# Performance work log

Hardware: AMD Instinct MI355X
Metric: run time of the kernel (lower is better)

## Reference

```python
import jax, jax.numpy as jnp
import numpy as np

N_E = 2048
E_DIM = 64
BETA = 0.25


def _l2_normalize(x, eps=1e-12):
    # matches F.normalize: x / clamp_min(||x||, eps)
    n = jnp.linalg.norm(x, axis=-1, keepdims=True)
    return x / jnp.maximum(n, eps)


def _cosine_sim(a, b, eps=1e-8):
    # matches torch.cosine_similarity(dim=-1)
    na = jnp.maximum(jnp.linalg.norm(a, axis=-1), eps)
    nb = jnp.maximum(jnp.linalg.norm(b, axis=-1), eps)
    return jnp.sum(a * b, axis=-1) / (na * nb)


def setup_inputs() -> dict:
    key = jax.random.key(0)
    k1, k2 = jax.random.split(key)
    z = jax.random.normal(k1, (16, 64, 64, E_DIM), dtype=jnp.float32)
    bound = 1.0 / np.sqrt(E_DIM)
    emb = jax.random.uniform(k2, (N_E, E_DIM), dtype=jnp.float32,
                             minval=-bound, maxval=bound)
    return {"z": z, "emb": emb}


def reference(z, emb):
    n_e, e_dim = emb.shape
    zf = z.reshape(-1, e_dim)                      # (N, C)
    N = zf.shape[0]

    cb = _l2_normalize(emb)                        # normalized codebook (n_e, C)
    # _d normalizes cb again (idempotent) and normalizes z
    z_norm = _l2_normalize(zf)
    d = jnp.matmul(z_norm, cb.T)                   # (N, n_e) cosine similarities

    idx = jnp.argmax(d, axis=1)                    # (N,)
    probs = jax.nn.softmax(d, axis=1)              # (N, n_e)

    # one-hot @ cb == gather
    z_q = cb[idx].reshape(z.shape)

    # commitment loss (stop-gradient semantics; forward value identical)
    sg = jax.lax.stop_gradient
    commit_loss = (1.0 - jnp.mean(_cosine_sim(z_q, sg(z)))) \
        + BETA * (1.0 - jnp.mean(_cosine_sim(sg(z_q), z)))

    # e_mean = mean of one-hot encodings == normalized codeword counts
    e_mean = jnp.zeros((n_e,), dtype=z.dtype).at[idx].add(1.0) / N

    p = jnp.mean(probs, axis=0)                    # (n_e,)
    kl_loss = jnp.sum(p * (jnp.log(p) - jnp.log(1.0 / n_e)))
    load_balancing_loss = jnp.sum(e_mean * p)

    z_q_st = z + sg(z_q - z)
    perplexity = jnp.exp(-jnp.sum(e_mean * jnp.log(e_mean + 1e-6)))

    return (z_q_st, commit_loss, kl_loss, load_balancing_loss, cb, perplexity)
```

## Files before the change

kernel.cpp:

```cpp
#include <hip/hip_runtime.h>
#include <math.h>

#define NROWS 65536
#define ED 64
#define NE 2048
#define TAU 3e-4f
#define LOG2E 1.44269504089f
#define LN2 0.69314718056f
#define TAUS (TAU * LOG2E)

typedef _Float16 f16x8 __attribute__((ext_vector_type(8)));
typedef float f32x4 __attribute__((ext_vector_type(4)));

#if __has_builtin(__builtin_amdgcn_exp2f)
__device__ __forceinline__ float fexp2(float x) { return __builtin_amdgcn_exp2f(x); }
#else
__device__ __forceinline__ float fexp2(float x) {
    float r;
    asm("v_exp_f32 %0, %1" : "=v"(r) : "v"(x));
    return r;
}
#endif

#define WS_CBH      0
#define WS_CBT      65536
#define WS_RINV     196608
#define WS_MROW     262144
#define WS_IDX      327680
#define WS_FLAGCNT  393216
#define WS_COUNTS   393232
#define WS_FLAGLIST 395280
#define WS_PSUM     460816
#define WS_MPART    462864
#define WS_PPART    462928

#define OUT_ZQ     0
#define OUT_COMMIT 4194304
#define OUT_KL     4194305
#define OUT_LB     4194306
#define OUT_CB     4194307
#define OUT_PERP   4325379

#define ZS_ZNORM   0
#define ZS_PM      2097152
#define ZS_PAUX    3145728
#define ZS_PSH     3670016

__global__ void k_cb(const float* __restrict__ emb, _Float16* __restrict__ cbh,
                     float* __restrict__ cbo, float* __restrict__ cbT) {
    int t = blockIdx.x * blockDim.x + threadIdx.x;
    int row = t >> 6;
    int lane = t & 63;
    if (row >= NE) return;
    float v = emb[row * ED + lane];
    float sq = v * v;
#pragma unroll
    for (int off = 32; off > 0; off >>= 1) sq += __shfl_xor(sq, off);
    float c = v * (1.0f / fmaxf(sqrtf(sq), 1e-12f));
    cbo[row * ED + lane] = c;
    cbh[row * ED + lane] = (_Float16)c;
    cbT[(size_t)lane * NE + row] = c;
}

__global__ void k_prep(const float* __restrict__ z, _Float16* __restrict__ znorm) {
    const int tid = threadIdx.x;
    const int lane = tid & 63;
    const int w = tid >> 6;
    const int row = blockIdx.x * 64 + w * 16 + (lane >> 2);
    const int q = lane & 3;
    const float4* zp = (const float4*)(z + (size_t)row * ED + q * 16);
    const float4 a = zp[0], b = zp[1], c = zp[2], d = zp[3];
    float sq = a.x*a.x + a.y*a.y + a.z*a.z + a.w*a.w
             + b.x*b.x + b.y*b.y + b.z*b.z + b.w*b.w
             + c.x*c.x + c.y*c.y + c.z*c.z + c.w*c.w
             + d.x*d.x + d.y*d.y + d.z*d.z + d.w*d.w;
    sq += __shfl_xor(sq, 1);
    sq += __shfl_xor(sq, 2);
    const float r = LOG2E / fmaxf(sqrtf(sq), 1e-12f);
    f16x8 h0, h1;
    h0[0]=(_Float16)(a.x*r); h0[1]=(_Float16)(a.y*r); h0[2]=(_Float16)(a.z*r); h0[3]=(_Float16)(a.w*r);
    h0[4]=(_Float16)(b.x*r); h0[5]=(_Float16)(b.y*r); h0[6]=(_Float16)(b.z*r); h0[7]=(_Float16)(b.w*r);
    h1[0]=(_Float16)(c.x*r); h1[1]=(_Float16)(c.y*r); h1[2]=(_Float16)(c.z*r); h1[3]=(_Float16)(c.w*r);
    h1[4]=(_Float16)(d.x*r); h1[5]=(_Float16)(d.y*r); h1[6]=(_Float16)(d.z*r); h1[7]=(_Float16)(d.w*r);
    f16x8* dst = (f16x8*)(znorm + (size_t)row * ED + q * 16);
    dst[0] = h0; dst[1] = h1;
}

__launch_bounds__(256, 3)
__global__ void k_s1(const _Float16* __restrict__ znorm, const _Float16* __restrict__ cbh,
                     float* __restrict__ pm, unsigned short* __restrict__ paux,
                     _Float16* __restrict__ psh) {
    const int tid = threadIdx.x;
    const int lane = tid & 63;
    const int w = tid >> 6;
    const int l15 = lane & 15;
    const int lg = lane >> 4;
    const int gw = blockIdx.x * 4 + w;
    const int g = gw & 15;
    const int split = gw >> 4;
    const int cwbase = g * 128;

    f16x8 af[8][2];
#pragma unroll
    for (int jf = 0; jf < 8; ++jf) {
        const _Float16* ap = cbh + (size_t)(cwbase + jf * 16 + l15) * ED + lg * 8;
        af[jf][0] = *(const f16x8*)(ap);
        af[jf][1] = *(const f16x8*)(ap + 32);
    }

    for (int t = 0; t < 4; ++t) {
        const int rbA = split * 128 + t * 32;
        const _Float16* bpA = znorm + (size_t)(rbA + l15) * ED + lg * 8;
        const _Float16* bpB = bpA + 16 * ED;
        const f16x8 bA0 = *(const f16x8*)(bpA);
        const f16x8 bA1 = *(const f16x8*)(bpA + 32);
        const f16x8 bB0 = *(const f16x8*)(bpB);
        const f16x8 bB1 = *(const f16x8*)(bpB + 32);
        float mA = -4.f, m2A = -4.f, sA0 = 0.f, sA1 = 0.f;
        float mB = -4.f, m2B = -4.f, sB0 = 0.f, sB1 = 0.f;
        int miA = 0, miB = 0;
#pragma unroll
        for (int jf = 0; jf < 8; ++jf) {
            f32x4 cA = (f32x4){0.f, 0.f, 0.f, 0.f};
            cA = __builtin_amdgcn_mfma_f32_16x16x32_f16(af[jf][0], bA0, cA, 0, 0, 0);
            cA = __builtin_amdgcn_mfma_f32_16x16x32_f16(af[jf][1], bA1, cA, 0, 0, 0);
            f32x4 cB = (f32x4){0.f, 0.f, 0.f, 0.f};
            cB = __builtin_amdgcn_mfma_f32_16x16x32_f16(af[jf][0], bB0, cB, 0, 0, 0);
            cB = __builtin_amdgcn_mfma_f32_16x16x32_f16(af[jf][1], bB1, cB, 0, 0, 0);
            const int cw0 = cwbase + jf * 16 + lg * 4;
#pragma unroll
            for (int i = 0; i < 4; ++i) {
                const float vA = cA[i];
                m2A = fmaxf(m2A, fminf(vA, mA));
                miA = (vA > mA) ? (cw0 + i) : miA;
                mA  = fmaxf(vA, mA);
                const float vB = cB[i];
                m2B = fmaxf(m2B, fminf(vB, mB));
                miB = (vB > mB) ? (cw0 + i) : miB;
                mB  = fmaxf(vB, mB);
                if (i & 1) { sA1 += fexp2(vA); sB1 += fexp2(vB); }
                else       { sA0 += fexp2(vA); sB0 += fexp2(vB); }
            }
        }
        float sA = sA0 + sA1, sB = sB0 + sB1;
#pragma unroll
        for (int d = 16; d <= 32; d <<= 1) {
            float om = __shfl_xor(mA, d);
            float om2 = __shfl_xor(m2A, d);
            int   oi = __shfl_xor(miA, d);
            sA += __shfl_xor(sA, d);
            float nm2 = fmaxf(fmaxf(m2A, om2), fminf(mA, om));
            bool take = (om > mA) || (om == mA && oi < miA);
            miA = take ? oi : miA;  mA = take ? om : mA;  m2A = nm2;
            om = __shfl_xor(mB, d);
            om2 = __shfl_xor(m2B, d);
            oi = __shfl_xor(miB, d);
            sB += __shfl_xor(sB, d);
            nm2 = fmaxf(fmaxf(m2B, om2), fminf(mB, om));
            take = (om > mB) || (om == mB && oi < miB);
            miB = take ? oi : miB;  mB = take ? om : mB;  m2B = nm2;
        }
        if (lane < 16) {
            int row = rbA + lane;
            pm[(size_t)g * NROWS + row] = mA;
            paux[(size_t)g * NROWS + row] =
                (unsigned short)(((mA - m2A < TAUS) ? 2048 : 0) | miA);
            psh[(size_t)g * NROWS + row] = (_Float16)sA;
            row += 16;
            pm[(size_t)g * NROWS + row] = mB;
            paux[(size_t)g * NROWS + row] =
                (unsigned short)(((mB - m2B < TAUS) ? 2048 : 0) | miB);
            psh[(size_t)g * NROWS + row] = (_Float16)sB;
        }
    }
}

__global__ void k_comb(const float* __restrict__ pm, const unsigned short* __restrict__ paux,
                       const _Float16* __restrict__ psh, float* __restrict__ rinv,
                       float* __restrict__ mrow, int* __restrict__ idxw,
                       int* __restrict__ flagcnt, int* __restrict__ flaglist,
                       float* __restrict__ counts) {
    const int row = blockIdx.x * 256 + threadIdx.x;
    float mg[16];
    unsigned short ax[16];
    float s = 0.f;
#pragma unroll
    for (int g = 0; g < 16; ++g) {
        mg[g] = pm[(size_t)g * NROWS + row];
        ax[g] = paux[(size_t)g * NROWS + row];
        s += (float)psh[(size_t)g * NROWS + row];
    }
    float bm = -4.f; int bi = 0;
#pragma unroll
    for (int g = 0; g < 16; ++g) {
        if (mg[g] > bm) { bm = mg[g]; bi = ax[g] & 2047; }
    }
    int near = 0; bool fl = false;
#pragma unroll
    for (int g = 0; g < 16; ++g) {
        const bool nr = (mg[g] >= bm - TAUS);
        near += nr ? 1 : 0;
        fl = fl || (nr && (ax[g] & 2048));
    }
    rinv[row] = 1.0f / s;
    mrow[row] = bm * LN2;
    idxw[row] = bi;
    if (fl || near >= 2) {
        int e = atomicAdd(flagcnt, 1);
        flaglist[e] = row;
    } else {
        atomicAdd(&counts[bi], 1.0f);
    }
}

__launch_bounds__(256, 3)
__global__ void k_s2(const _Float16* __restrict__ znorm, const _Float16* __restrict__ cbh,
                     const float* __restrict__ rinv, float* __restrict__ ppart) {
    const int tid = threadIdx.x;
    const int lane = tid & 63;
    const int w = tid >> 6;
    const int l15 = lane & 15;
    const int lg = lane >> 4;
    const int gw = blockIdx.x * 4 + w;
    const int cwg = gw & 31;
    const int split = gw >> 5;

    f16x8 bf[4][2];
#pragma unroll
    for (int jf = 0; jf < 4; ++jf) {
        const _Float16* bp = cbh + (size_t)(cwg * 64 + jf * 16 + l15) * ED + lg * 8;
        bf[jf][0] = *(const f16x8*)(bp);
        bf[jf][1] = *(const f16x8*)(bp + 32);
    }
    float pc[4] = {0.f, 0.f, 0.f, 0.f};

    for (int t = 0; t < 32; ++t) {
        const int rowbase = split * 512 + t * 16;
        const _Float16* ap = znorm + (size_t)(rowbase + l15) * ED + lg * 8;
        const f16x8 a0 = *(const f16x8*)(ap);
        const f16x8 a1 = *(const f16x8*)(ap + 32);
        const int r0 = rowbase + lg * 4;
        const float rv0 = rinv[r0], rv1 = rinv[r0 + 1];
        const float rv2 = rinv[r0 + 2], rv3 = rinv[r0 + 3];
#pragma unroll
        for (int jf = 0; jf < 4; ++jf) {
            f32x4 c = (f32x4){0.f, 0.f, 0.f, 0.f};
            c = __builtin_amdgcn_mfma_f32_16x16x32_f16(a0, bf[jf][0], c, 0, 0, 0);
            c = __builtin_amdgcn_mfma_f32_16x16x32_f16(a1, bf[jf][1], c, 0, 0, 0);
            pc[jf] += fexp2(c[0]) * rv0 + fexp2(c[1]) * rv1
                    + fexp2(c[2]) * rv2 + fexp2(c[3]) * rv3;
        }
    }
#pragma unroll
    for (int jf = 0; jf < 4; ++jf) {
        pc[jf] += __shfl_xor(pc[jf], 16);
        pc[jf] += __shfl_xor(pc[jf], 32);
    }
    if (lg == 0) {
        float* pp = ppart + (size_t)split * NE + cwg * 64;
#pragma unroll
        for (int jf = 0; jf < 4; ++jf) pp[jf * 16 + l15] = pc[jf];
    }
}

__global__ void k_zqg(const float* __restrict__ cb32, const int* __restrict__ idxw,
                      float* __restrict__ zq) {
    const int r = blockIdx.x * 16 + (threadIdx.x >> 4);
    const int q = threadIdx.x & 15;
    const int j = idxw[r];
    ((float4*)(zq + (size_t)r * ED))[q] = ((const float4*)(cb32 + (size_t)j * ED))[q];
}

__launch_bounds__(256, 2)
__global__ void k_recheck(const float* __restrict__ z, const float* __restrict__ cbT,
                          const float* __restrict__ cb32,
                          const int* __restrict__ flagcnt, const int* __restrict__ flaglist,
                          float* __restrict__ mrow, float* __restrict__ counts,
                          float* __restrict__ zq) {
    __shared__ float zn[8][ED];
    __shared__ int   rowids[8];
    __shared__ float rbv[8][4];
    __shared__ int   rbi[8][4];
    const int n = *flagcnt;
    const int tid = threadIdx.x, lane = tid & 63, wv = tid >> 6;
    for (int base = blockIdx.x * 8; base < n; base += 512 * 8) {
#pragma unroll
        for (int rr = wv * 2; rr < wv * 2 + 2; ++rr) {
            const int e = base + rr;
            int row = -1;
            float v = 0.f;
            if (e < n) { row = flaglist[e]; v = z[(size_t)row * ED + lane]; }
            float sq = v * v;
#pragma unroll
            for (int d = 32; d > 0; d >>= 1) sq += __shfl_xor(sq, d);
            zn[rr][lane] = v * (1.0f / fmaxf(sqrtf(sq), 1e-12f));
            if (lane == 0) rowids[rr] = row;
        }
        __syncthreads();
        float acc[8][8];
#pragma unroll
        for (int r = 0; r < 8; ++r)
#pragma unroll
            for (int q = 0; q < 8; ++q) acc[r][q] = 0.f;
        for (int k = 0; k < ED; ++k) {
            float cv[8];
            const float* cr = cbT + (size_t)k * NE + tid;
#pragma unroll
            for (int q = 0; q < 8; ++q) cv[q] = cr[q * 256];
#pragma unroll
            for (int r = 0; r < 8; ++r) {
                const float zk = zn[r][k];
#pragma unroll
                for (int q = 0; q < 8; ++q)
                    acc[r][q] = fmaf(zk, cv[q], acc[r][q]);
            }
        }
#pragma unroll
        for (int r = 0; r < 8; ++r) {
            float best = -2.f; int bj = 0;
#pragma unroll
            for (int q = 0; q < 8; ++q) {
                const float vv = acc[r][q];
                const int j = q * 256 + tid;
                bj = (vv > best) ? j : bj;
                best = fmaxf(vv, best);
            }
#pragma unroll
            for (int d = 1; d < 64; d <<= 1) {
                const float o = __shfl_xor(best, d);
                const int oj = __shfl_xor(bj, d);
                const bool tk = (o > best) || (o == best && oj < bj);
                best = tk ? o : best;
                bj = tk ? oj : bj;
            }
            if (lane == 0) { rbv[r][wv] = best; rbi[r][wv] = bj; }
        }
        __syncthreads();
        if (wv == 0 && lane < 8) {
            const int r = lane;
            float bv = rbv[r][0]; int bj = rbi[r][0];
#pragma unroll
            for (int u = 1; u < 4; ++u) {
                const float o = rbv[r][u]; const int oj = rbi[r][u];
                const bool tk = (o > bv) || (o == bv && oj < bj);
                bv = tk ? o : bv; bj = tk ? oj : bj;
            }
            rbi[r][0] = bj;
            const int row = rowids[r];
            if (row >= 0) {
                mrow[row] = bv;
                atomicAdd(&counts[bj], 1.0f);
            }
        }
        __syncthreads();
#pragma unroll
        for (int rr = wv * 2; rr < wv * 2 + 2; ++rr) {
            const int row = rowids[rr];
            if (row >= 0) {
                const int bj = rbi[rr][0];
                zq[(size_t)row * ED + lane] = cb32[(size_t)bj * ED + lane];
            }
        }
    }
}

__global__ void k_red(const float* __restrict__ ppart, const float* __restrict__ mrow,
                      float* __restrict__ psum, float* __restrict__ mpart) {
    const int tid = threadIdx.x;
    if (blockIdx.x < 8) {
        const int col = blockIdx.x * 256 + tid;
        float s = 0.f;
        for (int sl = 0; sl < 128; ++sl) s += ppart[(size_t)sl * NE + col];
        psum[col] = s;
    } else {
        __shared__ float lds[4];
        const int b = blockIdx.x - 8;
        const int r0 = b * 1024;
        float s = 0.f;
        for (int r = r0 + tid; r < r0 + 1024; r += 256) s += mrow[r];
        const int lane = tid & 63, wv = tid >> 6;
#pragma unroll
        for (int d = 32; d > 0; d >>= 1) s += __shfl_xor(s, d);
        if (lane == 0) lds[wv] = s;
        __syncthreads();
        if (tid == 0) mpart[b] = lds[0] + lds[1] + lds[2] + lds[3];
    }
}

__device__ __forceinline__ float block_reduce_1024(float v, float* lds, int lane, int wid) {
#pragma unroll
    for (int off = 32; off > 0; off >>= 1) v += __shfl_xor(v, off);
    if (lane == 0) lds[wid] = v;
    __syncthreads();
    float r = 0.f;
    if (wid == 0) {
        r = (lane < 16) ? lds[lane] : 0.f;
#pragma unroll
        for (int off = 8; off > 0; off >>= 1) r += __shfl_xor(r, off);
    }
    __syncthreads();
    return r;
}

__global__ void k_final(const float* __restrict__ counts, const float* __restrict__ psum,
                        const float* __restrict__ mpart, float* __restrict__ out) {
    __shared__ float lds[16];
    const int tid = threadIdx.x;
    const int lane = tid & 63, wid = tid >> 6;
    float sm = (tid < 64) ? mpart[tid] : 0.f;
    float kl = 0.f, lb = 0.f, H = 0.f;
    const float LOGNE = logf((float)NE);
    for (int j = tid; j < NE; j += 1024) {
        const float p = psum[j] * (1.0f / NROWS);
        const float em = counts[j] * (1.0f / NROWS);
        kl += p * (logf(p) + LOGNE);
        lb += em * p;
        H += em * logf(em + 1e-6f);
    }
    sm = block_reduce_1024(sm, lds, lane, wid);
    kl = block_reduce_1024(kl, lds, lane, wid);
    lb = block_reduce_1024(lb, lds, lane, wid);
    H  = block_reduce_1024(H,  lds, lane, wid);
    if (tid == 0) {
        out[OUT_COMMIT] = 1.25f * (1.0f - sm * (1.0f / NROWS));
        out[OUT_KL] = kl;
        out[OUT_LB] = lb;
        out[OUT_PERP] = expf(-H);
    }
}

extern "C" void kernel_launch(void* const* d_in, const int* in_sizes, int n_in,
                              void* d_out, int out_size, void* d_ws, size_t ws_size,
                              hipStream_t stream) {
    const float* z   = (const float*)d_in[0];
    const float* emb = (const float*)d_in[1];
    float* out = (float*)d_out;
    float* ws  = (float*)d_ws;

    _Float16* cbh  = (_Float16*)(ws + WS_CBH);
    float* cbT     = ws + WS_CBT;
    float* rinv    = ws + WS_RINV;
    float* mrowp   = ws + WS_MROW;
    int* idxw      = (int*)(ws + WS_IDX);
    int* flagcnt   = (int*)(ws + WS_FLAGCNT);
    int* flaglist  = (int*)(ws + WS_FLAGLIST);
    float* counts  = ws + WS_COUNTS;
    float* psum    = ws + WS_PSUM;
    float* mpart   = ws + WS_MPART;
    float* ppart   = ws + WS_PPART;
    float* cb32    = out + OUT_CB;
    float* zq      = out + OUT_ZQ;

    _Float16* znorm      = (_Float16*)(zq + ZS_ZNORM);
    float* pm            = zq + ZS_PM;
    unsigned short* paux = (unsigned short*)(zq + ZS_PAUX);
    _Float16* psh        = (_Float16*)(zq + ZS_PSH);

    hipMemsetAsync(flagcnt, 0, (16 + NE) * sizeof(float), stream);

    k_cb      <<<512, 256, 0, stream>>>(emb, cbh, cb32, cbT);
    k_prep    <<<1024, 256, 0, stream>>>(z, znorm);
    k_s1      <<<2048, 256, 0, stream>>>(znorm, cbh, pm, paux, psh);
    k_comb    <<<256, 256, 0, stream>>>(pm, paux, psh, rinv, mrowp, idxw,
                                        flagcnt, flaglist, counts);
    k_s2      <<<1024, 256, 0, stream>>>(znorm, cbh, rinv, ppart);
    k_zqg     <<<4096, 256, 0, stream>>>(cb32, idxw, zq);
    k_recheck <<<512, 256, 0, stream>>>(z, cbT, cb32, flagcnt, flaglist,
                                        mrowp, counts, zq);
    k_red     <<<72, 256, 0, stream>>>(ppart, mrowp, psum, mpart);
    k_final   <<<1, 1024, 0, stream>>>(counts, psum, mpart, out);
}
```

Measured before the change: 159.2 us.

## Merge small kernels into fewer launches and use med3 for second-max

Result: slower. 177.7 us (+11.7%).

```diff
diff --git a/kernel.cpp b/kernel.cpp
--- a/kernel.cpp
+++ b/kernel.cpp
@@ -21,6 +21,12 @@
     return r;
 }
 #endif
+
+__device__ __forceinline__ float fmed3(float a, float b, float c) {
+    float r;
+    asm("v_med3_f32 %0, %1, %2, %3" : "=v"(r) : "v"(a), "v"(b), "v"(c));
+    return r;
+}
 
 #define WS_CBH      0
 #define WS_CBT      65536
@@ -31,7 +37,6 @@
 #define WS_COUNTS   393232
 #define WS_FLAGLIST 395280
 #define WS_PSUM     460816
-#define WS_MPART    462864
 #define WS_PPART    462928
 
 #define OUT_ZQ     0
@@ -46,44 +51,45 @@
 #define ZS_PAUX    3145728
 #define ZS_PSH     3670016
 
-__global__ void k_cb(const float* __restrict__ emb, _Float16* __restrict__ cbh,
-                     float* __restrict__ cbo, float* __restrict__ cbT) {
-    int t = blockIdx.x * blockDim.x + threadIdx.x;
-    int row = t >> 6;
-    int lane = t & 63;
-    if (row >= NE) return;
-    float v = emb[row * ED + lane];
-    float sq = v * v;
-#pragma unroll
-    for (int off = 32; off > 0; off >>= 1) sq += __shfl_xor(sq, off);
-    float c = v * (1.0f / fmaxf(sqrtf(sq), 1e-12f));
-    cbo[row * ED + lane] = c;
-    cbh[row * ED + lane] = (_Float16)c;
-    cbT[(size_t)lane * NE + row] = c;
-}
-
-__global__ void k_prep(const float* __restrict__ z, _Float16* __restrict__ znorm) {
+__global__ void k_cbprep(const float* __restrict__ emb, _Float16* __restrict__ cbh,
+                         float* __restrict__ cbo, float* __restrict__ cbT,
+                         const float* __restrict__ z, _Float16* __restrict__ znorm) {
     const int tid = threadIdx.x;
     const int lane = tid & 63;
-    const int w = tid >> 6;
-    const int row = blockIdx.x * 64 + w * 16 + (lane >> 2);
-    const int q = lane & 3;
-    const float4* zp = (const float4*)(z + (size_t)row * ED + q * 16);
-    const float4 a = zp[0], b = zp[1], c = zp[2], d = zp[3];
-    float sq = a.x*a.x + a.y*a.y + a.z*a.z + a.w*a.w
-             + b.x*b.x + b.y*b.y + b.z*b.z + b.w*b.w
-             + c.x*c.x + c.y*c.y + c.z*c.z + c.w*c.w
-             + d.x*d.x + d.y*d.y + d.z*d.z + d.w*d.w;
-    sq += __shfl_xor(sq, 1);
-    sq += __shfl_xor(sq, 2);
-    const float r = LOG2E / fmaxf(sqrtf(sq), 1e-12f);
-    f16x8 h0, h1;
-    h0[0]=(_Float16)(a.x*r); h0[1]=(_Float16)(a.y*r); h0[2]=(_Float16)(a.z*r); h0[3]=(_Float16)(a.w*r);
-    h0[4]=(_Float16)(b.x*r); h0[5]=(_Float16)(b.y*r); h0[6]=(_Float16)(b.z*r); h0[7]=(_Float16)(b.w*r);
-    h1[0]=(_Float16)(c.x*r); h1[1]=(_Float16)(c.y*r); h1[2]=(_Float16)(c.z*r); h1[3]=(_Float16)(c.w*r);
-    h1[4]=(_Float16)(d.x*r); h1[5]=(_Float16)(d.y*r); h1[6]=(_Float16)(d.z*r); h1[7]=(_Float16)(d.w*r);
-    f16x8* dst = (f16x8*)(znorm + (size_t)row * ED + q * 16);
-    dst[0] = h0; dst[1] = h1;
+    if (blockIdx.x < 512) {
+        const int t = blockIdx.x * 256 + tid;
+        const int row = t >> 6;
+        if (row >= NE) return;
+        float v = emb[row * ED + lane];
+        float sq = v * v;
+#pragma unroll
+        for (int off = 32; off > 0; off >>= 1) sq += __shfl_xor(sq, off);
+        float c = v * (1.0f / fmaxf(sqrtf(sq), 1e-12f));
+        cbo[row * ED + lane] = c;
+        cbh[row * ED + lane] = (_Float16)c;
+        cbT[(size_t)lane * NE + row] = c;
+    } else {
+        const int bb = blockIdx.x - 512;
+        const int w = tid >> 6;
+        const int row = bb * 64 + w * 16 + (lane >> 2);
+        const int q = lane & 3;
+        const float4* zp = (const float4*)(z + (size_t)row * ED + q * 16);
+        const float4 a = zp[0], b = zp[1], c = zp[2], d = zp[3];
+        float sq = a.x*a.x + a.y*a.y + a.z*a.z + a.w*a.w
+                 + b.x*b.x + b.y*b.y + b.z*b.z + b.w*b.w
+                 + c.x*c.x + c.y*c.y + c.z*c.z + c.w*c.w
+                 + d.x*d.x + d.y*d.y + d.z*d.z + d.w*d.w;
+        sq += __shfl_xor(sq, 1);
+        sq += __shfl_xor(sq, 2);
+        const float r = LOG2E / fmaxf(sqrtf(sq), 1e-12f);
+        f16x8 h0, h1;
+        h0[0]=(_Float16)(a.x*r); h0[1]=(_Float16)(a.y*r); h0[2]=(_Float16)(a.z*r); h0[3]=(_Float16)(a.w*r);
+        h0[4]=(_Float16)(b.x*r); h0[5]=(_Float16)(b.y*r); h0[6]=(_Float16)(b.z*r); h0[7]=(_Float16)(b.w*r);
+        h1[0]=(_Float16)(c.x*r); h1[1]=(_Float16)(c.y*r); h1[2]=(_Float16)(c.z*r); h1[3]=(_Float16)(c.w*r);
+        h1[4]=(_Float16)(d.x*r); h1[5]=(_Float16)(d.y*r); h1[6]=(_Float16)(d.z*r); h1[7]=(_Float16)(d.w*r);
+        f16x8* dst = (f16x8*)(znorm + (size_t)row * ED + q * 16);
+        dst[0] = h0; dst[1] = h1;
+    }
 }
 
 __launch_bounds__(256, 3)
@@ -131,11 +137,11 @@
 #pragma unroll
             for (int i = 0; i < 4; ++i) {
                 const float vA = cA[i];
-                m2A = fmaxf(m2A, fminf(vA, mA));
+                m2A = fmed3(vA, m2A, mA);
                 miA = (vA > mA) ? (cw0 + i) : miA;
                 mA  = fmaxf(vA, mA);
                 const float vB = cB[i];
-                m2B = fmaxf(m2B, fminf(vB, mB));
+                m2B = fmed3(vB, m2B, mB);
                 miB = (vB > mB) ? (cw0 + i) : miB;
                 mB  = fmaxf(vB, mB);
                 if (i & 1) { sA1 += fexp2(vA); sB1 += fexp2(vB); }
@@ -204,8 +210,9 @@
     }
     rinv[row] = 1.0f / s;
     mrow[row] = bm * LN2;
-    idxw[row] = bi;
-    if (fl || near >= 2) {
+    const bool flagged = fl || near >= 2;
+    idxw[row] = flagged ? (bi | 0x80000000) : bi;
+    if (flagged) {
         int e = atomicAdd(flagcnt, 1);
         flaglist[e] = row;
     } else {
@@ -263,27 +270,36 @@
     }
 }
 
-__global__ void k_zqg(const float* __restrict__ cb32, const int* __restrict__ idxw,
-                      float* __restrict__ zq) {
-    const int r = blockIdx.x * 16 + (threadIdx.x >> 4);
-    const int q = threadIdx.x & 15;
-    const int j = idxw[r];
-    ((float4*)(zq + (size_t)r * ED))[q] = ((const float4*)(cb32 + (size_t)j * ED))[q];
-}
-
 __launch_bounds__(256, 2)
-__global__ void k_recheck(const float* __restrict__ z, const float* __restrict__ cbT,
-                          const float* __restrict__ cb32,
-                          const int* __restrict__ flagcnt, const int* __restrict__ flaglist,
-                          float* __restrict__ mrow, float* __restrict__ counts,
-                          float* __restrict__ zq) {
+__global__ void k_gr(const float* __restrict__ z, const float* __restrict__ cbT,
+                     const float* __restrict__ cb32, const int* __restrict__ idxw,
+                     const int* __restrict__ flagcnt, const int* __restrict__ flaglist,
+                     float* __restrict__ mrow, float* __restrict__ counts,
+                     float* __restrict__ zq, const float* __restrict__ ppart,
+                     float* __restrict__ psum) {
     __shared__ float zn[8][ED];
     __shared__ int   rowids[8];
     __shared__ float rbv[8][4];
     __shared__ int   rbi[8][4];
+    const int tid = threadIdx.x, lane = tid & 63, wv = tid >> 6;
+
+    if (blockIdx.x < 4096) {
+        const int r = blockIdx.x * 16 + (tid >> 4);
+        const int q = tid & 15;
+        const int j = idxw[r];
+        if (j >= 0)
+            ((float4*)(zq + (size_t)r * ED))[q] = ((const float4*)(cb32 + (size_t)j * ED))[q];
+        return;
+    }
+    if (blockIdx.x >= 4608) {
+        const int col = (blockIdx.x - 4608) * 256 + tid;
+        float s = 0.f;
+        for (int sl = 0; sl < 128; ++sl) s += ppart[(size_t)sl * NE + col];
+        psum[col] = s;
+        return;
+    }
     const int n = *flagcnt;
-    const int tid = threadIdx.x, lane = tid & 63, wv = tid >> 6;
-    for (int base = blockIdx.x * 8; base < n; base += 512 * 8) {
+    for (int base = (blockIdx.x - 4096) * 8; base < n; base += 512 * 8) {
 #pragma unroll
         for (int rr = wv * 2; rr < wv * 2 + 2; ++rr) {
             const int e = base + rr;
@@ -364,29 +380,6 @@
     }
 }
 
-__global__ void k_red(const float* __restrict__ ppart, const float* __restrict__ mrow,
-                      float* __restrict__ psum, float* __restrict__ mpart) {
-    const int tid = threadIdx.x;
-    if (blockIdx.x < 8) {
-        const int col = blockIdx.x * 256 + tid;
-        float s = 0.f;
-        for (int sl = 0; sl < 128; ++sl) s += ppart[(size_t)sl * NE + col];
-        psum[col] = s;
-    } else {
-        __shared__ float lds[4];
-        const int b = blockIdx.x - 8;
-        const int r0 = b * 1024;
-        float s = 0.f;
-        for (int r = r0 + tid; r < r0 + 1024; r += 256) s += mrow[r];
-        const int lane = tid & 63, wv = tid >> 6;
-#pragma unroll
-        for (int d = 32; d > 0; d >>= 1) s += __shfl_xor(s, d);
-        if (lane == 0) lds[wv] = s;
-        __syncthreads();
-        if (tid == 0) mpart[b] = lds[0] + lds[1] + lds[2] + lds[3];
-    }
-}
-
 __device__ __forceinline__ float block_reduce_1024(float v, float* lds, int lane, int wid) {
 #pragma unroll
     for (int off = 32; off > 0; off >>= 1) v += __shfl_xor(v, off);
@@ -403,11 +396,12 @@
 }
 
 __global__ void k_final(const float* __restrict__ counts, const float* __restrict__ psum,
-                        const float* __restrict__ mpart, float* __restrict__ out) {
+                        const float* __restrict__ mrow, float* __restrict__ out) {
     __shared__ float lds[16];
     const int tid = threadIdx.x;
     const int lane = tid & 63, wid = tid >> 6;
-    float sm = (tid < 64) ? mpart[tid] : 0.f;
+    float sm = 0.f;
+    for (int r = tid; r < NROWS; r += 1024) sm += mrow[r];
     float kl = 0.f, lb = 0.f, H = 0.f;
     const float LOGNE = logf((float)NE);
     for (int j = tid; j < NE; j += 1024) {
@@ -446,7 +440,6 @@
     int* flaglist  = (int*)(ws + WS_FLAGLIST);
     float* counts  = ws + WS_COUNTS;
     float* psum    = ws + WS_PSUM;
-    float* mpart   = ws + WS_MPART;
     float* ppart   = ws + WS_PPART;
     float* cb32    = out + OUT_CB;
     float* zq      = out + OUT_ZQ;
@@ -458,15 +451,12 @@
 
     hipMemsetAsync(flagcnt, 0, (16 + NE) * sizeof(float), stream);
 
-    k_cb      <<<512, 256, 0, stream>>>(emb, cbh, cb32, cbT);
-    k_prep    <<<1024, 256, 0, stream>>>(z, znorm);
-    k_s1      <<<2048, 256, 0, stream>>>(znorm, cbh, pm, paux, psh);
-    k_comb    <<<256, 256, 0, stream>>>(pm, paux, psh, rinv, mrowp, idxw,
-                                        flagcnt, flaglist, counts);
-    k_s2      <<<1024, 256, 0, stream>>>(znorm, cbh, rinv, ppart);
-    k_zqg     <<<4096, 256, 0, stream>>>(cb32, idxw, zq);
-    k_recheck <<<512, 256, 0, stream>>>(z, cbT, cb32, flagcnt, flaglist,
-                                        mrowp, counts, zq);
-    k_red     <<<72, 256, 0, stream>>>(ppart, mrowp, psum, mpart);
-    k_final   <<<1, 1024, 0, stream>>>(counts, psum, mpart, out);
-}
+    k_cbprep <<<1536, 256, 0, stream>>>(emb, cbh, cb32, cbT, z, znorm);
+    k_s1     <<<2048, 256, 0, stream>>>(znorm, cbh, pm, paux, psh);
+    k_comb   <<<256, 256, 0, stream>>>(pm, paux, psh, rinv, mrowp, idxw,
+                                       flagcnt, flaglist, counts);
+    k_s2     <<<1024, 256, 0, stream>>>(znorm, cbh, rinv, ppart);
+    k_gr     <<<4616, 256, 0, stream>>>(z, cbT, cb32, idxw, flagcnt, flaglist,
+                                        mrowp, counts, zq, ppart, psum);
+    k_final  <<<1, 1024, 0, stream>>>(counts, psum, mrowp, out);
+}
```
